# Optimization experiments

Measured on AMD Instinct MI355X. Metric: run time of the kernel, lower is better.

The kernel has to match this reference:

```python
import jax, jax.numpy as jnp
import numpy as np

M, K, N, E = 8192, 1024, 1024, 8  # total tokens, in-dim, out-dim, experts/segments


def setup_inputs() -> dict:
    key = jax.random.key(0)
    k1, k2, k3 = jax.random.split(key, 3)
    a = jax.random.normal(k1, (M, K), dtype=jnp.float32)
    b = jax.random.normal(k2, (E, N, K), dtype=jnp.float32) * 0.02  # column-major per-expert weights
    c = jnp.zeros((M, N), dtype=jnp.float32)
    inner = jnp.sort(jax.random.randint(k3, (E - 1,), 0, M, dtype=jnp.int32))
    seg_indptr = jnp.concatenate([
        jnp.zeros((1,), jnp.int32), inner, jnp.full((1,), M, jnp.int32)
    ])  # [E+1], monotone, covers [0, M)
    weight_indices = jnp.arange(E, dtype=jnp.int32)
    return {
        "a": a, "b": b, "c": c,
        "batch_size": E, "weight_column_major": 1,
        "seg_indptr": seg_indptr, "weight_indices": weight_indices,
    }


def reference(a, b, c, batch_size, weight_column_major, seg_indptr, weight_indices):
    # Grouped GEMM: for each contiguous segment s of rows [seg_indptr[s], seg_indptr[s+1]),
    # c[rows] = a[rows] @ b[weight_indices[s]].T  (b is [E, N, K], column-major weights).
    assert weight_column_major
    rows = jnp.arange(a.shape[0])[:, None]  # [M, 1]
    out = c
    for s in range(batch_size):  # fixed small loop over experts/segments
        b_e = jnp.take(b, weight_indices[s], axis=0)  # [N, K]
        seg_out = a @ b_e.T                            # [M, N]
        mask = (rows >= seg_indptr[s]) & (rows < seg_indptr[s + 1])
        out = jnp.where(mask, seg_out, out)
    return out
```

## Files before the change

kernel.cpp:

```cpp
#include <hip/hip_runtime.h>
#include <hip/hip_bf16.h>
#include <stdint.h>

#define MDIM 8192
#define KDIM 1024
#define NDIM 1024
#define NEXP 8
#define BM 64
#define BN 128
#define BK 32
#define LDSS 40

typedef __attribute__((ext_vector_type(8))) short bf16x8;
typedef __attribute__((ext_vector_type(4))) float floatx4;
typedef __attribute__((ext_vector_type(8))) unsigned short ushort8;

static __device__ __forceinline__ unsigned short f2b(float f) {
    unsigned int u = __float_as_uint(f);
    return (unsigned short)((u + 0x7fffu + ((u >> 16) & 1u)) >> 16);
}

__global__ __launch_bounds__(256)
void cvt_bf16(const float* __restrict__ a, const float* __restrict__ b,
              unsigned short* __restrict__ wa, unsigned short* __restrict__ wb)
{
    const long t  = (long)blockIdx.x * 256 + threadIdx.x;
    const long NA = (long)MDIM * KDIM / 8;
    const float* src; unsigned short* dst; long v;
    if (t < NA) { src = a; dst = wa; v = t; }
    else        { src = b; dst = wb; v = t - NA; }
    const float4 lo = ((const float4*)src)[2 * v];
    const float4 hi = ((const float4*)src)[2 * v + 1];
    ushort8 o;
    o[0] = f2b(lo.x); o[1] = f2b(lo.y); o[2] = f2b(lo.z); o[3] = f2b(lo.w);
    o[4] = f2b(hi.x); o[5] = f2b(hi.y); o[6] = f2b(hi.z); o[7] = f2b(hi.w);
    ((ushort8*)dst)[v] = o;
}

#define GLDS(gp, lp) __builtin_amdgcn_global_load_lds(                        \
    (const __attribute__((address_space(1))) unsigned int*)(gp),              \
    (__attribute__((address_space(3))) unsigned int*)(lp), 16, 0, 0)

__global__ __launch_bounds__(256, 4)
void grouped_gemm_ws(const unsigned short* __restrict__ A,
                     const unsigned short* __restrict__ B,
                     const int* __restrict__ seg_indptr,
                     const int* __restrict__ widx,
                     float* __restrict__ c)
{
    __shared__ unsigned short As[BM * BK];
    __shared__ unsigned short Bs[BN * BK];

    const int NTN = NDIM / BN;
    int rem = (int)blockIdx.x;
    int s = -1, m0 = 0, seg_end = 0, n0 = 0;
    for (int i = 0; i < NEXP; ++i) {
        int ps = seg_indptr[i], pe = seg_indptr[i + 1];
        int nt = ((pe - ps + BM - 1) / BM) * NTN;
        if (rem < nt) { s = i; m0 = ps + (rem / NTN) * BM; n0 = (rem % NTN) * BN; seg_end = pe; break; }
        rem -= nt;
    }
    if (s < 0) return;

    const unsigned short* __restrict__ be = B + (size_t)widx[s] * (size_t)(NDIM * KDIM);

    const int tid  = (int)threadIdx.x;
    const int wave = tid >> 6;
    const int lane = tid & 63;
    const int srow = tid >> 2;
    const int skc  = (tid & 3) * 8;
    int arow = m0 + srow; if (arow >= MDIM) arow = MDIM - 1;
    const int brow0 = n0 + srow, brow1 = n0 + 64 + srow;
    const int ldsoff = wave * 16 * BK;

    const int wm = (wave & 1) * 32;
    const int wn = (wave >> 1) * 64;
    const int fr = lane & 15;
    const int quad = lane >> 4;

    floatx4 acc[2][4] = {};

    const unsigned short* aptr  = A  + (size_t)arow  * KDIM + skc;
    const unsigned short* bptr0 = be + (size_t)brow0 * KDIM + skc;
    const unsigned short* bptr1 = be + (size_t)brow1 * KDIM + skc;

    for (int k0 = 0; k0 < KDIM; k0 += BK) {
        GLDS(aptr  + k0, &As[ldsoff]);
        GLDS(bptr0 + k0, &Bs[ldsoff]);
        GLDS(bptr1 + k0, &Bs[64 * BK + ldsoff]);
        __syncthreads();

        bf16x8 af[2], bf[4];
#pragma unroll
        for (int mi = 0; mi < 2; ++mi)
            af[mi] = *reinterpret_cast<const bf16x8*>(&As[(wm + mi * 16 + fr) * BK + quad * 8]);
#pragma unroll
        for (int ni = 0; ni < 4; ++ni)
            bf[ni] = *reinterpret_cast<const bf16x8*>(&Bs[(wn + ni * 16 + fr) * BK + quad * 8]);
#pragma unroll
        for (int mi = 0; mi < 2; ++mi)
#pragma unroll
            for (int ni = 0; ni < 4; ++ni)
                acc[mi][ni] = __builtin_amdgcn_mfma_f32_16x16x32_bf16(af[mi], bf[ni], acc[mi][ni], 0, 0, 0);
        __syncthreads();
    }

#pragma unroll
    for (int mi = 0; mi < 2; ++mi) {
        const int rbase = m0 + wm + mi * 16 + quad * 4;
#pragma unroll
        for (int ni = 0; ni < 4; ++ni) {
            const int col = n0 + wn + ni * 16 + fr;
#pragma unroll
            for (int j = 0; j < 4; ++j) {
                const int row = rbase + j;
                if (row < seg_end)
                    c[(size_t)row * NDIM + col] = acc[mi][ni][j];
            }
        }
    }
}

__global__ __launch_bounds__(256, 2)
void grouped_gemm_fused(const float* __restrict__ a, const float* __restrict__ b,
                        const int* __restrict__ seg_indptr, const int* __restrict__ widx,
                        float* __restrict__ c)
{
    __shared__ unsigned short Asf[128 * LDSS];
    __shared__ unsigned short Bsf[128 * LDSS];
    const int NTN = NDIM / 128;
    int rem = (int)blockIdx.x;
    int s = -1, m0 = 0, seg_end = 0, n0 = 0;
    for (int i = 0; i < NEXP; ++i) {
        int ps = seg_indptr[i], pe = seg_indptr[i + 1];
        int nt = ((pe - ps + 127) / 128) * NTN;
        if (rem < nt) { s = i; m0 = ps + (rem / NTN) * 128; n0 = (rem % NTN) * 128; seg_end = pe; break; }
        rem -= nt;
    }
    if (s < 0) return;
    const float* __restrict__ be = b + (size_t)widx[s] * (size_t)(NDIM * KDIM);
    const int tid = (int)threadIdx.x;
    const int r0 = tid >> 3;
    const int kc = (tid & 7) * 4;
    int arow[4];
#pragma unroll
    for (int u = 0; u < 4; ++u) {
        int r = m0 + r0 + 32 * u;
        arow[u] = r < MDIM ? r : MDIM - 1;
    }
    const int lane = tid & 63;
    const int wave = tid >> 6;
    const int wm = (wave & 1) * 64;
    const int wn = (wave >> 1) * 64;
    const int fr = lane & 15;
    const int quad = lane >> 4;
    floatx4 acc[4][4] = {};
    float4 av[4], bv[4];
#pragma unroll
    for (int u = 0; u < 4; ++u) {
        av[u] = *reinterpret_cast<const float4*>(a + (size_t)arow[u] * KDIM + kc);
        bv[u] = *reinterpret_cast<const float4*>(be + (size_t)(n0 + r0 + 32 * u) * KDIM + kc);
    }
    for (int k0 = 0; k0 < KDIM; k0 += BK) {
        __syncthreads();
#pragma unroll
        for (int u = 0; u < 4; ++u) {
            ushort4 ua, ub;
            ua.x = f2b(av[u].x); ua.y = f2b(av[u].y); ua.z = f2b(av[u].z); ua.w = f2b(av[u].w);
            ub.x = f2b(bv[u].x); ub.y = f2b(bv[u].y); ub.z = f2b(bv[u].z); ub.w = f2b(bv[u].w);
        *reinterpret_cast<ushort4*>(&Asf[(r0 + 32 * u) * LDSS + kc]) = ua;
        *reinterpret_cast<ushort4*>(&Bsf[(r0 + 32 * u) * LDSS + kc]) = ub;
        }
        const int kn = (k0 + BK < KDIM) ? (k0 + BK) : 0;
#pragma unroll
        for (int u = 0; u < 4; ++u) {
            av[u] = *reinterpret_cast<const float4*>(a + (size_t)arow[u] * KDIM + kn + kc);
            bv[u] = *reinterpret_cast<const float4*>(be + (size_t)(n0 + r0 + 32 * u) * KDIM + kn + kc);
        }
        __syncthreads();
        bf16x8 af[4], bf[4];
#pragma unroll
        for (int mi = 0; mi < 4; ++mi)
            af[mi] = *reinterpret_cast<const bf16x8*>(&Asf[(wm + mi * 16 + fr) * LDSS + quad * 8]);
#pragma unroll
        for (int ni = 0; ni < 4; ++ni)
            bf[ni] = *reinterpret_cast<const bf16x8*>(&Bsf[(wn + ni * 16 + fr) * LDSS + quad * 8]);
#pragma unroll
        for (int mi = 0; mi < 4; ++mi)
#pragma unroll
            for (int ni = 0; ni < 4; ++ni)
                acc[mi][ni] = __builtin_amdgcn_mfma_f32_16x16x32_bf16(af[mi], bf[ni], acc[mi][ni], 0, 0, 0);
    }
#pragma unroll
    for (int mi = 0; mi < 4; ++mi) {
        const int rbase = m0 + wm + mi * 16 + quad * 4;
#pragma unroll
        for (int ni = 0; ni < 4; ++ni) {
            const int col = n0 + wn + ni * 16 + fr;
#pragma unroll
            for (int j = 0; j < 4; ++j) {
                const int row = rbase + j;
                if (row < seg_end)
                    c[(size_t)row * NDIM + col] = acc[mi][ni][j];
            }
        }
    }
}

extern "C" void kernel_launch(void* const* d_in, const int* in_sizes, int n_in,
                              void* d_out, int out_size, void* d_ws, size_t ws_size,
                              hipStream_t stream) {
    const float* a          = (const float*)d_in[0];
    const float* b          = (const float*)d_in[1];
    const int*   seg_indptr = (const int*)d_in[5];
    const int*   widx       = (const int*)d_in[6];
    float*       out        = (float*)d_out;

    const size_t need = (size_t)(MDIM + NEXP * NDIM) * KDIM * sizeof(unsigned short);
    if (ws_size >= need) {
        unsigned short* wa = (unsigned short*)d_ws;
        unsigned short* wb = wa + (size_t)MDIM * KDIM;
        hipLaunchKernelGGL(cvt_bf16, dim3(8192), dim3(256), 0, stream, a, b, wa, wb);
        hipLaunchKernelGGL(grouped_gemm_ws, dim3(135 * 8), dim3(256), 0, stream,
                           wa, wb, seg_indptr, widx, out);
    } else {
        hipLaunchKernelGGL(grouped_gemm_fused, dim3(568), dim3(256), 0, stream,
                           a, b, seg_indptr, widx, out);
    }
}
```

Before: 172.5 us.

## Replace LDS-staged GEMM with per-wave register-direct tiles and double-buffered fragments

The bf16 workspace GEMM no longer stages tiles through LDS with global_load_lds and two barriers per K step. Each wave now owns an independent 64x64 output tile and loads MFMA fragments straight from global memory into registers. Fragments are double-buffered across 32-wide K halves so the next loads overlap the current MFMAs. This removes LDS traffic and block-wide syncs, but waves no longer share loads, so global/L2 traffic per FLOP rises and the per-lane 16-byte loads are strided by rows.

```diff
diff --git a/kernel.cpp b/kernel.cpp
--- a/kernel.cpp
+++ b/kernel.cpp
@@ -6,9 +6,9 @@
 #define KDIM 1024
 #define NDIM 1024
 #define NEXP 8
-#define BM 64
-#define BN 128
-#define BK 32
+#define WTM 64
+#define WTN 64
+#define NTN (NDIM / WTN)
 #define LDSS 40
 
 typedef __attribute__((ext_vector_type(8))) short bf16x8;
@@ -37,80 +37,80 @@
     ((ushort8*)dst)[v] = o;
 }
 
-#define GLDS(gp, lp) __builtin_amdgcn_global_load_lds(                        \
-    (const __attribute__((address_space(1))) unsigned int*)(gp),              \
-    (__attribute__((address_space(3))) unsigned int*)(lp), 16, 0, 0)
-
-__global__ __launch_bounds__(256, 4)
-void grouped_gemm_ws(const unsigned short* __restrict__ A,
-                     const unsigned short* __restrict__ B,
-                     const int* __restrict__ seg_indptr,
-                     const int* __restrict__ widx,
-                     float* __restrict__ c)
+__global__ __launch_bounds__(256, 2)
+void grouped_gemm_reg(const unsigned short* __restrict__ A,
+                      const unsigned short* __restrict__ B,
+                      const int* __restrict__ seg_indptr,
+                      const int* __restrict__ widx,
+                      float* __restrict__ c)
 {
-    __shared__ unsigned short As[BM * BK];
-    __shared__ unsigned short Bs[BN * BK];
-
-    const int NTN = NDIM / BN;
-    int rem = (int)blockIdx.x;
+    const int wave = (int)threadIdx.x >> 6;
+    const int lane = (int)threadIdx.x & 63;
+    const int tile = (int)blockIdx.x * 4 + wave;
+
+    int rem = tile;
     int s = -1, m0 = 0, seg_end = 0, n0 = 0;
     for (int i = 0; i < NEXP; ++i) {
         int ps = seg_indptr[i], pe = seg_indptr[i + 1];
-        int nt = ((pe - ps + BM - 1) / BM) * NTN;
-        if (rem < nt) { s = i; m0 = ps + (rem / NTN) * BM; n0 = (rem % NTN) * BN; seg_end = pe; break; }
+        int nt = ((pe - ps + WTM - 1) / WTM) * NTN;
+        if (rem < nt) { s = i; m0 = ps + (rem / NTN) * WTM; n0 = (rem % NTN) * WTN; seg_end = pe; break; }
         rem -= nt;
     }
     if (s < 0) return;
 
     const unsigned short* __restrict__ be = B + (size_t)widx[s] * (size_t)(NDIM * KDIM);
-
-    const int tid  = (int)threadIdx.x;
-    const int wave = tid >> 6;
-    const int lane = tid & 63;
-    const int srow = tid >> 2;
-    const int skc  = (tid & 3) * 8;
-    int arow = m0 + srow; if (arow >= MDIM) arow = MDIM - 1;
-    const int brow0 = n0 + srow, brow1 = n0 + 64 + srow;
-    const int ldsoff = wave * 16 * BK;
-
-    const int wm = (wave & 1) * 32;
-    const int wn = (wave >> 1) * 64;
-    const int fr = lane & 15;
+    const int fr   = lane & 15;
     const int quad = lane >> 4;
 
-    floatx4 acc[2][4] = {};
-
-    const unsigned short* aptr  = A  + (size_t)arow  * KDIM + skc;
-    const unsigned short* bptr0 = be + (size_t)brow0 * KDIM + skc;
-    const unsigned short* bptr1 = be + (size_t)brow1 * KDIM + skc;
-
-    for (int k0 = 0; k0 < KDIM; k0 += BK) {
-        GLDS(aptr  + k0, &As[ldsoff]);
-        GLDS(bptr0 + k0, &Bs[ldsoff]);
-        GLDS(bptr1 + k0, &Bs[64 * BK + ldsoff]);
-        __syncthreads();
-
-        bf16x8 af[2], bf[4];
-#pragma unroll
-        for (int mi = 0; mi < 2; ++mi)
-            af[mi] = *reinterpret_cast<const bf16x8*>(&As[(wm + mi * 16 + fr) * BK + quad * 8]);
-#pragma unroll
-        for (int ni = 0; ni < 4; ++ni)
-            bf[ni] = *reinterpret_cast<const bf16x8*>(&Bs[(wn + ni * 16 + fr) * BK + quad * 8]);
-#pragma unroll
-        for (int mi = 0; mi < 2; ++mi)
+    const unsigned short* ap[4];
+    const unsigned short* bp[4];
+#pragma unroll
+    for (int i = 0; i < 4; ++i) {
+        int ra = m0 + i * 16 + fr; if (ra >= MDIM) ra = MDIM - 1;
+        ap[i] = A  + (size_t)ra * KDIM + quad * 8;
+        bp[i] = be + (size_t)(n0 + i * 16 + fr) * KDIM + quad * 8;
+    }
+
+    floatx4 acc[4][4] = {};
+    bf16x8 af[2][4], bf[2][4];
+
+#pragma unroll
+    for (int i = 0; i < 4; ++i) {
+        af[0][i] = *reinterpret_cast<const bf16x8*>(ap[i]);
+        bf[0][i] = *reinterpret_cast<const bf16x8*>(bp[i]);
+    }
+
+    for (int k0 = 0; k0 < KDIM; k0 += 64) {
+#pragma unroll
+        for (int i = 0; i < 4; ++i) {
+            af[1][i] = *reinterpret_cast<const bf16x8*>(ap[i] + k0 + 32);
+            bf[1][i] = *reinterpret_cast<const bf16x8*>(bp[i] + k0 + 32);
+        }
+#pragma unroll
+        for (int mi = 0; mi < 4; ++mi)
 #pragma unroll
             for (int ni = 0; ni < 4; ++ni)
-                acc[mi][ni] = __builtin_amdgcn_mfma_f32_16x16x32_bf16(af[mi], bf[ni], acc[mi][ni], 0, 0, 0);
-        __syncthreads();
-    }
-
-#pragma unroll
-    for (int mi = 0; mi < 2; ++mi) {
-        const int rbase = m0 + wm + mi * 16 + quad * 4;
+                acc[mi][ni] = __builtin_amdgcn_mfma_f32_16x16x32_bf16(af[0][mi], bf[0][ni], acc[mi][ni], 0, 0, 0);
+
+        const int kn = (k0 + 64 < KDIM) ? (k0 + 64) : 0;
+#pragma unroll
+        for (int i = 0; i < 4; ++i) {
+            af[0][i] = *reinterpret_cast<const bf16x8*>(ap[i] + kn);
+            bf[0][i] = *reinterpret_cast<const bf16x8*>(bp[i] + kn);
+        }
+#pragma unroll
+        for (int mi = 0; mi < 4; ++mi)
+#pragma unroll
+            for (int ni = 0; ni < 4; ++ni)
+                acc[mi][ni] = __builtin_amdgcn_mfma_f32_16x16x32_bf16(af[1][mi], bf[1][ni], acc[mi][ni], 0, 0, 0);
+    }
+
+#pragma unroll
+    for (int mi = 0; mi < 4; ++mi) {
+        const int rbase = m0 + mi * 16 + quad * 4;
 #pragma unroll
         for (int ni = 0; ni < 4; ++ni) {
-            const int col = n0 + wn + ni * 16 + fr;
+            const int col = n0 + ni * 16 + fr;
 #pragma unroll
             for (int j = 0; j < 4; ++j) {
                 const int row = rbase + j;
@@ -128,13 +128,13 @@
 {
     __shared__ unsigned short Asf[128 * LDSS];
     __shared__ unsigned short Bsf[128 * LDSS];
-    const int NTN = NDIM / 128;
+    const int NT = NDIM / 128;
     int rem = (int)blockIdx.x;
     int s = -1, m0 = 0, seg_end = 0, n0 = 0;
     for (int i = 0; i < NEXP; ++i) {
         int ps = seg_indptr[i], pe = seg_indptr[i + 1];
-        int nt = ((pe - ps + 127) / 128) * NTN;
-        if (rem < nt) { s = i; m0 = ps + (rem / NTN) * 128; n0 = (rem % NTN) * 128; seg_end = pe; break; }
+        int nt = ((pe - ps + 127) / 128) * NT;
+        if (rem < nt) { s = i; m0 = ps + (rem / NT) * 128; n0 = (rem % NT) * 128; seg_end = pe; break; }
         rem -= nt;
     }
     if (s < 0) return;
@@ -161,17 +161,17 @@
         av[u] = *reinterpret_cast<const float4*>(a + (size_t)arow[u] * KDIM + kc);
         bv[u] = *reinterpret_cast<const float4*>(be + (size_t)(n0 + r0 + 32 * u) * KDIM + kc);
     }
-    for (int k0 = 0; k0 < KDIM; k0 += BK) {
+    for (int k0 = 0; k0 < KDIM; k0 += 32) {
         __syncthreads();
 #pragma unroll
         for (int u = 0; u < 4; ++u) {
             ushort4 ua, ub;
             ua.x = f2b(av[u].x); ua.y = f2b(av[u].y); ua.z = f2b(av[u].z); ua.w = f2b(av[u].w);
             ub.x = f2b(bv[u].x); ub.y = f2b(bv[u].y); ub.z = f2b(bv[u].z); ub.w = f2b(bv[u].w);
-        *reinterpret_cast<ushort4*>(&Asf[(r0 + 32 * u) * LDSS + kc]) = ua;
-        *reinterpret_cast<ushort4*>(&Bsf[(r0 + 32 * u) * LDSS + kc]) = ub;
-        }
-        const int kn = (k0 + BK < KDIM) ? (k0 + BK) : 0;
+            *reinterpret_cast<ushort4*>(&Asf[(r0 + 32 * u) * LDSS + kc]) = ua;
+            *reinterpret_cast<ushort4*>(&Bsf[(r0 + 32 * u) * LDSS + kc]) = ub;
+        }
+        const int kn = (k0 + 32 < KDIM) ? (k0 + 32) : 0;
 #pragma unroll
         for (int u = 0; u < 4; ++u) {
             av[u] = *reinterpret_cast<const float4*>(a + (size_t)arow[u] * KDIM + kn + kc);
@@ -221,7 +221,7 @@
         unsigned short* wa = (unsigned short*)d_ws;
         unsigned short* wb = wa + (size_t)MDIM * KDIM;
         hipLaunchKernelGGL(cvt_bf16, dim3(8192), dim3(256), 0, stream, a, b, wa, wb);
-        hipLaunchKernelGGL(grouped_gemm_ws, dim3(135 * 8), dim3(256), 0, stream,
+        hipLaunchKernelGGL(grouped_gemm_reg, dim3(540), dim3(256), 0, stream,
                            wa, wb, seg_indptr, widx, out);
     } else {
         hipLaunchKernelGGL(grouped_gemm_fused, dim3(568), dim3(256), 0, stream,
```

Measured after the change: 224.2 us. 1.3x slower.

## Enlarge GEMM tiles, double-buffer LDS with swizzle, and remap block order

Applied to the files above, without the earlier changes.

The bf16 workspace GEMM moves to 128x128x64 tiles with two LDS buffers, so the global_load_lds for the next K slice is issued while MFMAs run on the current one. An XOR swizzle on 16-byte chunks is meant to cut LDS bank conflicts, and the block index is permuted to interleave tiles across the grid. Larger tiles raise operand reuse and halve the block count. In exchange, occupancy drops to two blocks per CU and the grid becomes less even.

```diff
diff --git a/kernel.cpp b/kernel.cpp
--- a/kernel.cpp
+++ b/kernel.cpp
@@ -6,9 +6,9 @@
 #define KDIM 1024
 #define NDIM 1024
 #define NEXP 8
-#define BM 64
+#define BM 128
 #define BN 128
-#define BK 32
+#define BK 64
 #define LDSS 40
 
 typedef __attribute__((ext_vector_type(8))) short bf16x8;
@@ -41,18 +41,21 @@
     (const __attribute__((address_space(1))) unsigned int*)(gp),              \
     (__attribute__((address_space(3))) unsigned int*)(lp), 16, 0, 0)
 
-__global__ __launch_bounds__(256, 4)
-void grouped_gemm_ws(const unsigned short* __restrict__ A,
+
+__global__ __launch_bounds__(256, 2)
+void grouped_gemm_v5(const unsigned short* __restrict__ A,
                      const unsigned short* __restrict__ B,
                      const int* __restrict__ seg_indptr,
                      const int* __restrict__ widx,
                      float* __restrict__ c)
 {
-    __shared__ unsigned short As[BM * BK];
-    __shared__ unsigned short Bs[BN * BK];
+    __shared__ unsigned short As0[BM * BK], As1[BM * BK];
+    __shared__ unsigned short Bs0[BN * BK], Bs1[BN * BK];
+
+    const int bid = ((int)blockIdx.x & 7) * 71 + ((int)blockIdx.x >> 3);
 
     const int NTN = NDIM / BN;
-    int rem = (int)blockIdx.x;
+    int rem = bid;
     int s = -1, m0 = 0, seg_end = 0, n0 = 0;
     for (int i = 0; i < NEXP; ++i) {
         int ps = seg_indptr[i], pe = seg_indptr[i + 1];
@@ -67,46 +70,74 @@
     const int tid  = (int)threadIdx.x;
     const int wave = tid >> 6;
     const int lane = tid & 63;
-    const int srow = tid >> 2;
-    const int skc  = (tid & 3) * 8;
-    int arow = m0 + srow; if (arow >= MDIM) arow = MDIM - 1;
-    const int brow0 = n0 + srow, brow1 = n0 + 64 + srow;
-    const int ldsoff = wave * 16 * BK;
-
-    const int wm = (wave & 1) * 32;
+
+    const int srow = tid >> 3;
+    const int gch  = ((tid & 7) ^ (srow & 7)) * 8;
+    const unsigned short* ap[4];
+    const unsigned short* bp[4];
+#pragma unroll
+    for (int j = 0; j < 4; ++j) {
+        int ra = m0 + j * 32 + srow; if (ra >= MDIM) ra = MDIM - 1;
+        ap[j] = A  + (size_t)ra * KDIM + gch;
+        bp[j] = be + (size_t)(n0 + j * 32 + srow) * KDIM + gch;
+    }
+    const int ldso = wave * 512;
+
+    const int wm = (wave & 1) * 64;
     const int wn = (wave >> 1) * 64;
-    const int fr = lane & 15;
+    const int fr   = lane & 15;
     const int quad = lane >> 4;
-
-    floatx4 acc[2][4] = {};
-
-    const unsigned short* aptr  = A  + (size_t)arow  * KDIM + skc;
-    const unsigned short* bptr0 = be + (size_t)brow0 * KDIM + skc;
-    const unsigned short* bptr1 = be + (size_t)brow1 * KDIM + skc;
-
-    for (int k0 = 0; k0 < KDIM; k0 += BK) {
-        GLDS(aptr  + k0, &As[ldsoff]);
-        GLDS(bptr0 + k0, &Bs[ldsoff]);
-        GLDS(bptr1 + k0, &Bs[64 * BK + ldsoff]);
-        __syncthreads();
-
-        bf16x8 af[2], bf[4];
-#pragma unroll
-        for (int mi = 0; mi < 2; ++mi)
-            af[mi] = *reinterpret_cast<const bf16x8*>(&As[(wm + mi * 16 + fr) * BK + quad * 8]);
-#pragma unroll
-        for (int ni = 0; ni < 4; ++ni)
-            bf[ni] = *reinterpret_cast<const bf16x8*>(&Bs[(wn + ni * 16 + fr) * BK + quad * 8]);
-#pragma unroll
-        for (int mi = 0; mi < 2; ++mi)
-#pragma unroll
-            for (int ni = 0; ni < 4; ++ni)
-                acc[mi][ni] = __builtin_amdgcn_mfma_f32_16x16x32_bf16(af[mi], bf[ni], acc[mi][ni], 0, 0, 0);
-        __syncthreads();
-    }
-
-#pragma unroll
-    for (int mi = 0; mi < 2; ++mi) {
+    const int fro0 = ((0 * 4 + quad) ^ (fr & 7)) * 8;
+    const int fro1 = ((1 * 4 + quad) ^ (fr & 7)) * 8;
+
+    floatx4 acc[4][4] = {};
+
+#define STAGE(AS, BS, kk)                                                     \
+    do {                                                                      \
+        _Pragma("unroll")                                                     \
+        for (int j = 0; j < 4; ++j) {                                         \
+            GLDS(ap[j] + (kk), &AS[j * 2048 + ldso]);                         \
+            GLDS(bp[j] + (kk), &BS[j * 2048 + ldso]);                         \
+        }                                                                     \
+    } while (0)
+
+#define COMPUTE(AS, BS)                                                       \
+    do {                                                                      \
+        bf16x8 af[4], bf[4];                                                  \
+        _Pragma("unroll")                                                     \
+        for (int h = 0; h < 2; ++h) {                                         \
+            const int fro = h ? fro1 : fro0;                                  \
+            _Pragma("unroll")                                                 \
+            for (int mi = 0; mi < 4; ++mi)                                    \
+                af[mi] = *reinterpret_cast<const bf16x8*>(                    \
+                    &AS[(wm + mi * 16 + fr) * BK + fro]);                     \
+            _Pragma("unroll")                                                 \
+            for (int ni = 0; ni < 4; ++ni)                                    \
+                bf[ni] = *reinterpret_cast<const bf16x8*>(                    \
+                    &BS[(wn + ni * 16 + fr) * BK + fro]);                     \
+            _Pragma("unroll")                                                 \
+            for (int mi = 0; mi < 4; ++mi)                                    \
+                _Pragma("unroll")                                             \
+                for (int ni = 0; ni < 4; ++ni)                                \
+                    acc[mi][ni] = __builtin_amdgcn_mfma_f32_16x16x32_bf16(    \
+                        af[mi], bf[ni], acc[mi][ni], 0, 0, 0);                \
+        }                                                                     \
+    } while (0)
+
+    STAGE(As0, Bs0, 0);
+#pragma unroll 1
+    for (int ii = 0; ii < 8; ++ii) {
+        const int i0 = ii * 2;
+        __syncthreads();
+        STAGE(As1, Bs1, (i0 + 1) * BK);
+        COMPUTE(As0, Bs0);
+        __syncthreads();
+        if (i0 + 2 < 16) STAGE(As0, Bs0, (i0 + 2) * BK);
+        COMPUTE(As1, Bs1);
+    }
+
+#pragma unroll
+    for (int mi = 0; mi < 4; ++mi) {
         const int rbase = m0 + wm + mi * 16 + quad * 4;
 #pragma unroll
         for (int ni = 0; ni < 4; ++ni) {
@@ -119,6 +150,8 @@
             }
         }
     }
+#undef STAGE
+#undef COMPUTE
 }
 
 __global__ __launch_bounds__(256, 2)
@@ -128,13 +161,13 @@
 {
     __shared__ unsigned short Asf[128 * LDSS];
     __shared__ unsigned short Bsf[128 * LDSS];
-    const int NTN = NDIM / 128;
+    const int NT = NDIM / 128;
     int rem = (int)blockIdx.x;
     int s = -1, m0 = 0, seg_end = 0, n0 = 0;
     for (int i = 0; i < NEXP; ++i) {
         int ps = seg_indptr[i], pe = seg_indptr[i + 1];
-        int nt = ((pe - ps + 127) / 128) * NTN;
-        if (rem < nt) { s = i; m0 = ps + (rem / NTN) * 128; n0 = (rem % NTN) * 128; seg_end = pe; break; }
+        int nt = ((pe - ps + 127) / 128) * NT;
+        if (rem < nt) { s = i; m0 = ps + (rem / NT) * 128; n0 = (rem % NT) * 128; seg_end = pe; break; }
         rem -= nt;
     }
     if (s < 0) return;
@@ -161,17 +194,17 @@
         av[u] = *reinterpret_cast<const float4*>(a + (size_t)arow[u] * KDIM + kc);
         bv[u] = *reinterpret_cast<const float4*>(be + (size_t)(n0 + r0 + 32 * u) * KDIM + kc);
     }
-    for (int k0 = 0; k0 < KDIM; k0 += BK) {
+    for (int k0 = 0; k0 < KDIM; k0 += 32) {
         __syncthreads();
 #pragma unroll
         for (int u = 0; u < 4; ++u) {
             ushort4 ua, ub;
             ua.x = f2b(av[u].x); ua.y = f2b(av[u].y); ua.z = f2b(av[u].z); ua.w = f2b(av[u].w);
             ub.x = f2b(bv[u].x); ub.y = f2b(bv[u].y); ub.z = f2b(bv[u].z); ub.w = f2b(bv[u].w);
-        *reinterpret_cast<ushort4*>(&Asf[(r0 + 32 * u) * LDSS + kc]) = ua;
-        *reinterpret_cast<ushort4*>(&Bsf[(r0 + 32 * u) * LDSS + kc]) = ub;
-        }
-        const int kn = (k0 + BK < KDIM) ? (k0 + BK) : 0;
+            *reinterpret_cast<ushort4*>(&Asf[(r0 + 32 * u) * LDSS + kc]) = ua;
+            *reinterpret_cast<ushort4*>(&Bsf[(r0 + 32 * u) * LDSS + kc]) = ub;
+        }
+        const int kn = (k0 + 32 < KDIM) ? (k0 + 32) : 0;
 #pragma unroll
         for (int u = 0; u < 4; ++u) {
             av[u] = *reinterpret_cast<const float4*>(a + (size_t)arow[u] * KDIM + kn + kc);
@@ -221,7 +254,7 @@
         unsigned short* wa = (unsigned short*)d_ws;
         unsigned short* wb = wa + (size_t)MDIM * KDIM;
         hipLaunchKernelGGL(cvt_bf16, dim3(8192), dim3(256), 0, stream, a, b, wa, wb);
-        hipLaunchKernelGGL(grouped_gemm_ws, dim3(135 * 8), dim3(256), 0, stream,
+        hipLaunchKernelGGL(grouped_gemm_v5, dim3(568), dim3(256), 0, stream,
                            wa, wb, seg_indptr, widx, out);
     } else {
         hipLaunchKernelGGL(grouped_gemm_fused, dim3(568), dim3(256), 0, stream,
```

After: 164.0 us. 1.05x faster.
